# Performance work log

Hardware: AMD Instinct MI355X
Metric: run time of the kernel (lower is better)

The kernel has to match this reference:

```python
import jax, jax.numpy as jnp
import numpy as np


def setup_inputs() -> dict:
    key = jax.random.key(0)
    k1, k2, k3 = jax.random.split(key, 3)
    x = jax.random.normal(k1, (16, 64, 256, 256), dtype=jnp.float32)
    # Conv2d(2, 1, kernel_size=7, padding=3): weight [out=1, in=2, 7, 7], bias [1]
    fan_in = 2 * 7 * 7
    bound = 1.0 / np.sqrt(fan_in)
    conv_w = jax.random.uniform(k2, (1, 2, 7, 7), jnp.float32, -bound, bound)
    conv_b = jax.random.uniform(k3, (1,), jnp.float32, -bound, bound)
    return {"x": x, "conv_w": conv_w, "conv_b": conv_b}


def reference(x, conv_w, conv_b):
    # x: [B, C, H, W]
    avg_out = jnp.mean(x, axis=1, keepdims=True)          # [B,1,H,W]
    max_out = jnp.max(x, axis=1, keepdims=True)           # [B,1,H,W]
    att = jnp.concatenate([avg_out, max_out], axis=1)     # [B,2,H,W]
    att = jax.lax.conv_general_dilated(
        att, conv_w,
        window_strides=(1, 1),
        padding=((3, 3), (3, 3)),
        dimension_numbers=("NCHW", "OIHW", "NCHW"),
    ) + conv_b.reshape(1, 1, 1, 1)                         # [B,1,H,W]
    att = jax.nn.sigmoid(att)
    return x * att
```

## Files before the change

kernel.cpp:

```cpp
#include <hip/hip_runtime.h>
#include <math.h>

#define BB   16
#define CC   64
#define HH_  256
#define WW_  256
#define HW   (HH_ * WW_)
#define CHW  (CC * HW)
#define NPIX (BB * HW)
#define N4   (NPIX / 4)

typedef float vfloat4 __attribute__((ext_vector_type(4)));

__global__ __launch_bounds__(256) void pool_kernel(const float* __restrict__ x,
                                                   float* __restrict__ avgp,
                                                   float* __restrict__ maxp) {
    int idx = blockIdx.x * blockDim.x + threadIdx.x;
    int b  = idx >> 14;
    int p4 = idx & 16383;

    const float4* x4 = (const float4*)x + (size_t)b * (CHW / 4) + p4;

    float4 s = {0.f, 0.f, 0.f, 0.f};
    float4 m = {-INFINITY, -INFINITY, -INFINITY, -INFINITY};
    #pragma unroll 8
    for (int c = 0; c < CC; ++c) {
        float4 v = x4[c * (HW / 4)];
        s.x += v.x; s.y += v.y; s.z += v.z; s.w += v.w;
        m.x = fmaxf(m.x, v.x); m.y = fmaxf(m.y, v.y);
        m.z = fmaxf(m.z, v.z); m.w = fmaxf(m.w, v.w);
    }
    const float inv = 1.0f / 64.0f;
    float4 a = {s.x * inv, s.y * inv, s.z * inv, s.w * inv};
    ((float4*)avgp)[idx] = a;
    ((float4*)maxp)[idx] = m;
}

__global__ __launch_bounds__(256) void conv_scale_kernel(const float* __restrict__ x,
                                                         const float* __restrict__ avgp,
                                                         const float* __restrict__ maxp,
                                                         const float* __restrict__ cw,
                                                         const float* __restrict__ cb,
                                                         float* __restrict__ out) {
    __shared__ float sw[99];
    if (threadIdx.x < 99)
        sw[threadIdx.x] = (threadIdx.x < 98) ? cw[threadIdx.x] : cb[0];
    __syncthreads();

    int bid = gridDim.x - 1 - blockIdx.x;
    int idx = bid * blockDim.x + threadIdx.x;
    int b   = idx >> 14;
    int p4  = idx & 16383;
    int pix = p4 << 2;
    int h   = pix >> 8;
    int q   = p4 & 63;

    const float* ap = avgp + b * HW;
    const float* mp = maxp + b * HW;

    float bias = sw[98];
    float acc0 = bias, acc1 = bias, acc2 = bias, acc3 = bias;

    for (int dy = -3; dy <= 3; ++dy) {
        int hh = h + dy;
        if (hh < 0 || hh >= HH_) continue;
        const float4* a4 = (const float4*)(ap + hh * WW_);
        const float4* m4 = (const float4*)(mp + hh * WW_);
        const float4 z = {0.f, 0.f, 0.f, 0.f};
        float4 aL = (q > 0)  ? a4[q - 1] : z;
        float4 aC = a4[q];
        float4 aR = (q < 63) ? a4[q + 1] : z;
        float4 mL = (q > 0)  ? m4[q - 1] : z;
        float4 mC = m4[q];
        float4 mR = (q < 63) ? m4[q + 1] : z;
        float av[12] = {aL.x, aL.y, aL.z, aL.w, aC.x, aC.y, aC.z, aC.w, aR.x, aR.y, aR.z, aR.w};
        float mv[12] = {mL.x, mL.y, mL.z, mL.w, mC.x, mC.y, mC.z, mC.w, mR.x, mR.y, mR.z, mR.w};

        const float* wr = sw + (dy + 3) * 7;
        #pragma unroll
        for (int kx = 0; kx < 7; ++kx) {
            float wa = wr[kx];
            float wm = wr[49 + kx];
            int t = 1 + kx;
            acc0 = fmaf(av[t + 0], wa, acc0);  acc0 = fmaf(mv[t + 0], wm, acc0);
            acc1 = fmaf(av[t + 1], wa, acc1);  acc1 = fmaf(mv[t + 1], wm, acc1);
            acc2 = fmaf(av[t + 2], wa, acc2);  acc2 = fmaf(mv[t + 2], wm, acc2);
            acc3 = fmaf(av[t + 3], wa, acc3);  acc3 = fmaf(mv[t + 3], wm, acc3);
        }
    }

    float att0 = 1.f / (1.f + __expf(-acc0));
    float att1 = 1.f / (1.f + __expf(-acc1));
    float att2 = 1.f / (1.f + __expf(-acc2));
    float att3 = 1.f / (1.f + __expf(-acc3));

    const vfloat4* xb = (const vfloat4*)x + (size_t)b * (CHW / 4) + p4;
    vfloat4*       ob = (vfloat4*)out     + (size_t)b * (CHW / 4) + p4;
    #pragma unroll 4
    for (int c = 0; c < CC; ++c) {
        vfloat4 v = __builtin_nontemporal_load(xb + c * (HW / 4));
        vfloat4 r;
        r.x = v.x * att0; r.y = v.y * att1; r.z = v.z * att2; r.w = v.w * att3;
        __builtin_nontemporal_store(r, ob + c * (HW / 4));
    }
}

extern "C" void kernel_launch(void* const* d_in, const int* in_sizes, int n_in,
                              void* d_out, int out_size, void* d_ws, size_t ws_size,
                              hipStream_t stream) {
    const float* x  = (const float*)d_in[0];
    const float* cw = (const float*)d_in[1];
    const float* cb = (const float*)d_in[2];
    float* out = (float*)d_out;

    float* avgp = (float*)d_ws;
    float* maxp = avgp + NPIX;

    dim3 block(256);
    dim3 grid(N4 / 256);
    pool_kernel<<<grid, block, 0, stream>>>(x, avgp, maxp);
    conv_scale_kernel<<<grid, block, 0, stream>>>(x, avgp, maxp, cw, cb, out);
}
```

Baseline: 493.6 us.

## Fuse channel pooling, conv and scaling into one banded kernel with LDS halo

Replaces the separate pooling and conv+scale kernels with a single kernel where each block owns an 8-row band of one image. It recomputes channel mean/max for the band plus a 3-row halo into shared memory, applies the 7x7 conv from LDS, and rescales x. This removes the workspace round-trip and a kernel launch, but recomputes halo rows (1.75x pooling reads) and launches only 512 blocks, which may limit memory-level parallelism.

```diff
diff --git a/kernel.cpp b/kernel.cpp
--- a/kernel.cpp
+++ b/kernel.cpp
@@ -7,101 +7,108 @@
 #define WW_  256
 #define HW   (HH_ * WW_)
 #define CHW  (CC * HW)
-#define NPIX (BB * HW)
-#define N4   (NPIX / 4)
+#define BH   8
+#define HALO 3
+#define PR   (BH + 2*HALO)
+#define NBANDS (HH_ / BH)
+#define NBLK (BB * NBANDS)
 
 typedef float vfloat4 __attribute__((ext_vector_type(4)));
 
-__global__ __launch_bounds__(256) void pool_kernel(const float* __restrict__ x,
-                                                   float* __restrict__ avgp,
-                                                   float* __restrict__ maxp) {
-    int idx = blockIdx.x * blockDim.x + threadIdx.x;
-    int b  = idx >> 14;
-    int p4 = idx & 16383;
+__global__ __launch_bounds__(256) void fused_kernel(const float* __restrict__ x,
+                                                    const float* __restrict__ cw,
+                                                    const float* __restrict__ cb,
+                                                    float* __restrict__ out) {
+    __shared__ float sw[99];
+    __shared__ float ap[PR][WW_];
+    __shared__ float mp[PR][WW_];
 
-    const float4* x4 = (const float4*)x + (size_t)b * (CHW / 4) + p4;
+    const int tid = threadIdx.x;
+    if (tid < 99) sw[tid] = (tid < 98) ? cw[tid] : cb[0];
 
-    float4 s = {0.f, 0.f, 0.f, 0.f};
-    float4 m = {-INFINITY, -INFINITY, -INFINITY, -INFINITY};
-    #pragma unroll 8
-    for (int c = 0; c < CC; ++c) {
-        float4 v = x4[c * (HW / 4)];
-        s.x += v.x; s.y += v.y; s.z += v.z; s.w += v.w;
-        m.x = fmaxf(m.x, v.x); m.y = fmaxf(m.y, v.y);
-        m.z = fmaxf(m.z, v.z); m.w = fmaxf(m.w, v.w);
+    const int bid  = blockIdx.x;
+    const int b    = bid >> 5;
+    const int band = bid & (NBANDS - 1);
+    const int R0   = band * BH;
+
+    const float4* xb4 = (const float4*)x + (size_t)b * (CHW / 4);
+
+    for (int j = tid; j < PR * 64; j += 256) {
+        const int i   = j >> 6;
+        const int q   = j & 63;
+        const int row = R0 - HALO + i;
+        float4 a = {0.f, 0.f, 0.f, 0.f};
+        float4 m = {0.f, 0.f, 0.f, 0.f};
+        if (row >= 0 && row < HH_) {
+            const float4* p = xb4 + row * 64 + q;
+            float4 s  = {0.f, 0.f, 0.f, 0.f};
+            float4 mm = {-INFINITY, -INFINITY, -INFINITY, -INFINITY};
+            #pragma unroll 8
+            for (int c = 0; c < CC; ++c) {
+                float4 v = p[c * (HW / 4)];
+                s.x += v.x; s.y += v.y; s.z += v.z; s.w += v.w;
+                mm.x = fmaxf(mm.x, v.x); mm.y = fmaxf(mm.y, v.y);
+                mm.z = fmaxf(mm.z, v.z); mm.w = fmaxf(mm.w, v.w);
+            }
+            const float inv = 1.0f / 64.0f;
+            a.x = s.x * inv; a.y = s.y * inv; a.z = s.z * inv; a.w = s.w * inv;
+            m = mm;
+        }
+        *(float4*)&ap[i][q * 4] = a;
+        *(float4*)&mp[i][q * 4] = m;
     }
-    const float inv = 1.0f / 64.0f;
-    float4 a = {s.x * inv, s.y * inv, s.z * inv, s.w * inv};
-    ((float4*)avgp)[idx] = a;
-    ((float4*)maxp)[idx] = m;
-}
-
-__global__ __launch_bounds__(256) void conv_scale_kernel(const float* __restrict__ x,
-                                                         const float* __restrict__ avgp,
-                                                         const float* __restrict__ maxp,
-                                                         const float* __restrict__ cw,
-                                                         const float* __restrict__ cb,
-                                                         float* __restrict__ out) {
-    __shared__ float sw[99];
-    if (threadIdx.x < 99)
-        sw[threadIdx.x] = (threadIdx.x < 98) ? cw[threadIdx.x] : cb[0];
     __syncthreads();
 
-    int bid = gridDim.x - 1 - blockIdx.x;
-    int idx = bid * blockDim.x + threadIdx.x;
-    int b   = idx >> 14;
-    int p4  = idx & 16383;
-    int pix = p4 << 2;
-    int h   = pix >> 8;
-    int q   = p4 & 63;
+    const float bias = sw[98];
 
-    const float* ap = avgp + b * HW;
-    const float* mp = maxp + b * HW;
+    for (int s = 0; s < 2; ++s) {
+        const int k   = tid + s * 256;
+        const int rl  = k >> 6;
+        const int q   = k & 63;
+        const int row = R0 + rl;
 
-    float bias = sw[98];
-    float acc0 = bias, acc1 = bias, acc2 = bias, acc3 = bias;
+        float acc0 = bias, acc1 = bias, acc2 = bias, acc3 = bias;
+        #pragma unroll
+        for (int dy = -3; dy <= 3; ++dy) {
+            const int li = rl + HALO + dy;
+            const float4* a4 = (const float4*)&ap[li][0];
+            const float4* m4 = (const float4*)&mp[li][0];
+            const float4 z = {0.f, 0.f, 0.f, 0.f};
+            float4 aL = (q > 0)  ? a4[q - 1] : z;
+            float4 aC = a4[q];
+            float4 aR = (q < 63) ? a4[q + 1] : z;
+            float4 mL = (q > 0)  ? m4[q - 1] : z;
+            float4 mC = m4[q];
+            float4 mR = (q < 63) ? m4[q + 1] : z;
+            float av[12] = {aL.x,aL.y,aL.z,aL.w, aC.x,aC.y,aC.z,aC.w, aR.x,aR.y,aR.z,aR.w};
+            float mv[12] = {mL.x,mL.y,mL.z,mL.w, mC.x,mC.y,mC.z,mC.w, mR.x,mR.y,mR.z,mR.w};
+            const float* wr = sw + (dy + 3) * 7;
+            #pragma unroll
+            for (int kx = 0; kx < 7; ++kx) {
+                float wa = wr[kx];
+                float wm = wr[49 + kx];
+                int t = 1 + kx;
+                acc0 = fmaf(av[t + 0], wa, acc0);  acc0 = fmaf(mv[t + 0], wm, acc0);
+                acc1 = fmaf(av[t + 1], wa, acc1);  acc1 = fmaf(mv[t + 1], wm, acc1);
+                acc2 = fmaf(av[t + 2], wa, acc2);  acc2 = fmaf(mv[t + 2], wm, acc2);
+                acc3 = fmaf(av[t + 3], wa, acc3);  acc3 = fmaf(mv[t + 3], wm, acc3);
+            }
+        }
 
-    for (int dy = -3; dy <= 3; ++dy) {
-        int hh = h + dy;
-        if (hh < 0 || hh >= HH_) continue;
-        const float4* a4 = (const float4*)(ap + hh * WW_);
-        const float4* m4 = (const float4*)(mp + hh * WW_);
-        const float4 z = {0.f, 0.f, 0.f, 0.f};
-        float4 aL = (q > 0)  ? a4[q - 1] : z;
-        float4 aC = a4[q];
-        float4 aR = (q < 63) ? a4[q + 1] : z;
-        float4 mL = (q > 0)  ? m4[q - 1] : z;
-        float4 mC = m4[q];
-        float4 mR = (q < 63) ? m4[q + 1] : z;
-        float av[12] = {aL.x, aL.y, aL.z, aL.w, aC.x, aC.y, aC.z, aC.w, aR.x, aR.y, aR.z, aR.w};
-        float mv[12] = {mL.x, mL.y, mL.z, mL.w, mC.x, mC.y, mC.z, mC.w, mR.x, mR.y, mR.z, mR.w};
+        const float att0 = 1.f / (1.f + __expf(-acc0));
+        const float att1 = 1.f / (1.f + __expf(-acc1));
+        const float att2 = 1.f / (1.f + __expf(-acc2));
+        const float att3 = 1.f / (1.f + __expf(-acc3));
 
-        const float* wr = sw + (dy + 3) * 7;
-        #pragma unroll
-        for (int kx = 0; kx < 7; ++kx) {
-            float wa = wr[kx];
-            float wm = wr[49 + kx];
-            int t = 1 + kx;
-            acc0 = fmaf(av[t + 0], wa, acc0);  acc0 = fmaf(mv[t + 0], wm, acc0);
-            acc1 = fmaf(av[t + 1], wa, acc1);  acc1 = fmaf(mv[t + 1], wm, acc1);
-            acc2 = fmaf(av[t + 2], wa, acc2);  acc2 = fmaf(mv[t + 2], wm, acc2);
-            acc3 = fmaf(av[t + 3], wa, acc3);  acc3 = fmaf(mv[t + 3], wm, acc3);
+        const vfloat4* xr = (const vfloat4*)x  + (size_t)b * (CHW / 4) + row * 64 + q;
+        vfloat4*       ow = (vfloat4*)out      + (size_t)b * (CHW / 4) + row * 64 + q;
+        #pragma unroll 4
+        for (int c = 0; c < CC; ++c) {
+            vfloat4 v = __builtin_nontemporal_load(xr + c * (HW / 4));
+            vfloat4 r;
+            r.x = v.x * att0; r.y = v.y * att1; r.z = v.z * att2; r.w = v.w * att3;
+            __builtin_nontemporal_store(r, ow + c * (HW / 4));
         }
-    }
-
-    float att0 = 1.f / (1.f + __expf(-acc0));
-    float att1 = 1.f / (1.f + __expf(-acc1));
-    float att2 = 1.f / (1.f + __expf(-acc2));
-    float att3 = 1.f / (1.f + __expf(-acc3));
-
-    const vfloat4* xb = (const vfloat4*)x + (size_t)b * (CHW / 4) + p4;
-    vfloat4*       ob = (vfloat4*)out     + (size_t)b * (CHW / 4) + p4;
-    #pragma unroll 4
-    for (int c = 0; c < CC; ++c) {
-        vfloat4 v = __builtin_nontemporal_load(xb + c * (HW / 4));
-        vfloat4 r;
-        r.x = v.x * att0; r.y = v.y * att1; r.z = v.z * att2; r.w = v.w * att3;
-        __builtin_nontemporal_store(r, ob + c * (HW / 4));
     }
 }
 
@@ -113,11 +120,5 @@
     const float* cb = (const float*)d_in[2];
     float* out = (float*)d_out;
 
-    float* avgp = (float*)d_ws;
-    float* maxp = avgp + NPIX;
-
-    dim3 block(256);
-    dim3 grid(N4 / 256);
-    pool_kernel<<<grid, block, 0, stream>>>(x, avgp, maxp);
-    conv_scale_kernel<<<grid, block, 0, stream>>>(x, avgp, maxp, cw, cb, out);
+    fused_kernel<<<dim3(NBLK), dim3(256), 0, stream>>>(x, cw, cb, out);
 }
```

Result: slower. 532.0 us (+7.8%).
